# Kernel optimization log

Hardware: AMD Instinct MI355X
Metric: run time of the kernel (lower is better)

Reference implementation:

```python
import jax, jax.numpy as jnp
import numpy as np

EPS = 1e-12  # torch F.normalize eps


def setup_inputs() -> dict:
    key = jax.random.key(0)
    k1, k2, k3 = jax.random.split(key, 3)
    B, C, N, E, EMB = 128, 16, 128, 4, 16
    OUT = EMB // E  # Linear(emb_sz, emb_sz // num_edges)
    x = jax.random.normal(k1, (B, C, N, EMB), dtype=jnp.float32)
    A = jax.random.uniform(k2, (E, N, N), dtype=jnp.float32)  # non-negative adjacency
    # per-edge-type Linear weights, stored [E, in, out] so y = x @ W[e]
    W = jax.random.normal(k3, (E, EMB, OUT), dtype=jnp.float32) * (1.0 / np.sqrt(EMB))
    return {"x": x, "A": A, "W": W}


def reference(x, A, W):
    # F.normalize(A[e], dim=0): L2-normalize each column -> norm over rows (axis=1 of [E,N,N])
    col_norm = jnp.sqrt(jnp.sum(A * A, axis=1, keepdims=True))  # [E,1,N]
    An = A / jnp.maximum(col_norm, EPS)                         # [E,N,N]
    # x.transpose(3,2) @ An[e] then transpose back:
    # out[e,b,c,m,f] = sum_n x[b,c,n,f] * An[e,n,m]
    msg = jnp.einsum('bcnf,enm->ebcmf', x, An)                  # [E,B,C,N,EMB]
    # per-edge Linear (bias=False) + relu
    h = jax.nn.relu(jnp.einsum('ebcmf,efo->ebcmo', msg, W))     # [E,B,C,N,OUT]
    E_, B, C, N, O = h.shape
    # torch.cat([h_0, h_1, ...], axis=1) -> [B, E*C, N, OUT]
    out = jnp.transpose(h, (1, 0, 2, 3, 4)).reshape(B, E_ * C, N, O)
    return out
```

## Files before the change

kernel.cpp:

```cpp
#include <hip/hip_runtime.h>
#include <math.h>

#define EPSN 1e-12f

typedef __attribute__((ext_vector_type(8))) __bf16 bf16x8;
typedef __attribute__((ext_vector_type(8))) short short8;
typedef __attribute__((ext_vector_type(4))) float floatx4;

static __device__ __forceinline__ unsigned short f2bf(float f) {
    return __builtin_bit_cast(unsigned short, (__bf16)f);
}

__global__ __launch_bounds__(256)
void prep_kernel(const float* __restrict__ A, unsigned short* __restrict__ At) {
    __shared__ float Asub[128][33];
    __shared__ float red[8][32];
    __shared__ float rnv[32];
    const int t  = threadIdx.x;
    const int e  = blockIdx.x >> 2;
    const int m0 = (blockIdx.x & 3) * 32;
    const float* Ae = A + e * 16384 + m0;

    #pragma unroll
    for (int i = 0; i < 16; ++i) {
        int idx = t + i * 256;
        int n = idx >> 5, ml = idx & 31;
        Asub[n][ml] = Ae[n * 128 + ml];
    }
    __syncthreads();

    {
        int ml = t & 31, g = t >> 5;
        float s = 0.f;
        #pragma unroll
        for (int j = 0; j < 16; ++j) {
            float v = Asub[g * 16 + j][ml];
            s += v * v;
        }
        red[g][ml] = s;
    }
    __syncthreads();
    if (t < 32) {
        float s = 0.f;
        #pragma unroll
        for (int g = 0; g < 8; ++g) s += red[g][t];
        rnv[t] = 1.0f / fmaxf(sqrtf(s), EPSN);
    }
    __syncthreads();

    {
        int ml = t >> 3;
        int n0 = (t & 7) * 16;
        float r = rnv[ml];
        unsigned short hs[16];
        #pragma unroll
        for (int j = 0; j < 16; ++j)
            hs[j] = f2bf(Asub[n0 + j][ml] * r);
        uint4* dst = (uint4*)(At + ((size_t)(e * 128 + m0 + ml) * 128 + n0));
        dst[0] = *(const uint4*)&hs[0];
        dst[1] = *(const uint4*)&hs[8];
    }
}

__global__ __launch_bounds__(256)
void gcn_mfma_kernel(const float* __restrict__ x, const float* __restrict__ W,
                     const unsigned short* __restrict__ At,
                     float* __restrict__ out) {
    __shared__ __align__(16) unsigned short xw[8192];

    const int t   = threadIdx.x;
    const int bc0 = blockIdx.x * 4;

    float4 xf[2][4];
    int bcl_[2], n_[2];
    #pragma unroll
    for (int p = 0; p < 2; ++p) {
        int pair = t + p * 256;
        int bcl = pair >> 7, n = pair & 127;
        bcl_[p] = bcl; n_[p] = n;
        const float4* xp = (const float4*)(x + ((size_t)(bc0 + bcl) * 128 + n) * 16);
        xf[p][0] = xp[0]; xf[p][1] = xp[1]; xf[p][2] = xp[2]; xf[p][3] = xp[3];
    }
    #pragma unroll 1
    for (int e = 0; e < 4; ++e) {
        float4 We[16];
        const float4* wp = (const float4*)(W + e * 64);
        #pragma unroll
        for (int f = 0; f < 16; ++f) We[f] = wp[f];
        #pragma unroll
        for (int p = 0; p < 2; ++p) {
            float a0 = 0.f, a1 = 0.f, a2 = 0.f, a3 = 0.f;
            #pragma unroll
            for (int f = 0; f < 16; ++f) {
                float xv = ((const float*)&xf[p][f >> 2])[f & 3];
                a0 += xv * We[f].x; a1 += xv * We[f].y;
                a2 += xv * We[f].z; a3 += xv * We[f].w;
            }
            float av[4] = {a0, a1, a2, a3};
            int n = n_[p];
            #pragma unroll
            for (int o = 0; o < 4; ++o) {
                int r = bcl_[p] * 4 + o;
                int byteoff = (((e * 16 + r) << 8) + (n << 1)) ^ ((r & 7) << 4);
                *(unsigned short*)((char*)xw + byteoff) = f2bf(av[o]);
            }
        }
    }
    __syncthreads();

    const int e  = t >> 6;
    const int l  = t & 63;
    const int lr = l & 15;
    const int lg = l >> 4;

    bf16x8 afrag[4];
    #pragma unroll
    for (int ks = 0; ks < 4; ++ks) {
        int n0 = ks * 32 + lg * 8;
        int byteoff = (((e * 16 + lr) << 8) + (n0 << 1)) ^ ((lr & 7) << 4);
        short8 v = *(const short8*)((const char*)xw + byteoff);
        afrag[ks] = __builtin_bit_cast(bf16x8, v);
    }

    floatx4 acc[8];
    #pragma unroll
    for (int mt = 0; mt < 8; ++mt) acc[mt] = (floatx4){0.f, 0.f, 0.f, 0.f};

    const unsigned short* Ate = At + (size_t)e * 16384;
    #pragma unroll
    for (int mt = 0; mt < 8; ++mt) {
        int m = mt * 16 + lr;
        bf16x8 bfrag[4];
        #pragma unroll
        for (int ks = 0; ks < 4; ++ks) {
            int n0 = ks * 32 + lg * 8;
            short8 v = *(const short8*)(Ate + m * 128 + n0);
            bfrag[ks] = __builtin_bit_cast(bf16x8, v);
        }
        #pragma unroll
        for (int ks = 0; ks < 4; ++ks)
            acc[mt] = __builtin_amdgcn_mfma_f32_16x16x32_bf16(
                afrag[ks], bfrag[ks], acc[mt], 0, 0, 0);
    }

    const int bc = bc0 + lg, b = bc >> 4, c = bc & 15;
    float4* outp = (float4*)out + ((size_t)(b * 64 + e * 16 + c) * 128);
    #pragma unroll
    for (int mt = 0; mt < 8; ++mt) {
        int m = mt * 16 + lr;
        float4 o4;
        o4.x = fmaxf(acc[mt][0], 0.f);
        o4.y = fmaxf(acc[mt][1], 0.f);
        o4.z = fmaxf(acc[mt][2], 0.f);
        o4.w = fmaxf(acc[mt][3], 0.f);
        outp[m] = o4;
    }
}

extern "C" void kernel_launch(void* const* d_in, const int* in_sizes, int n_in,
                              void* d_out, int out_size, void* d_ws, size_t ws_size,
                              hipStream_t stream) {
    const float* x = (const float*)d_in[0];
    const float* A = (const float*)d_in[1];
    const float* W = (const float*)d_in[2];
    float* out = (float*)d_out;
    unsigned short* At = (unsigned short*)d_ws;

    prep_kernel<<<16, 256, 0, stream>>>(A, At);
    gcn_mfma_kernel<<<512, 256, 0, stream>>>(x, W, At, out);
}
```

Measured before the change: 23.10 us.

## Fuse adjacency normalization into main kernel with inter-block flag synchronization

Merges the separate prep kernel into the main MFMA kernel: the first 16 blocks normalize and transpose A into the workspace, then publish a release flag, and all blocks spin on those flags before reading At. Blocks are doubled to 512 threads handling 8 bc rows each, with each wave covering two row tiles and half the m range, so B fragments are reused across two MFMAs. This removes one kernel launch and overlaps the prep with the x@W stage, at the cost of an added memset and spin-wait that depends on the producer blocks being resident.

```diff
diff --git a/kernel.cpp b/kernel.cpp
--- a/kernel.cpp
+++ b/kernel.cpp
@@ -2,6 +2,7 @@
 #include <math.h>
 
 #define EPSN 1e-12f
+#define MAGIC 0x5A17C0DEu
 
 typedef __attribute__((ext_vector_type(8))) __bf16 bf16x8;
 typedef __attribute__((ext_vector_type(8))) short short8;
@@ -11,76 +12,79 @@
     return __builtin_bit_cast(unsigned short, (__bf16)f);
 }
 
-__global__ __launch_bounds__(256)
-void prep_kernel(const float* __restrict__ A, unsigned short* __restrict__ At) {
-    __shared__ float Asub[128][33];
-    __shared__ float red[8][32];
+__global__ __launch_bounds__(512, 2)
+void gcn_fused_kernel(const float* __restrict__ x, const float* __restrict__ A,
+                      const float* __restrict__ W,
+                      unsigned short* __restrict__ At, unsigned* __restrict__ flags,
+                      float* __restrict__ out) {
+    __shared__ __align__(16) unsigned char smem[32768];
+    __shared__ float red[16][32];
     __shared__ float rnv[32];
-    const int t  = threadIdx.x;
-    const int e  = blockIdx.x >> 2;
-    const int m0 = (blockIdx.x & 3) * 32;
-    const float* Ae = A + e * 16384 + m0;
-
-    #pragma unroll
-    for (int i = 0; i < 16; ++i) {
-        int idx = t + i * 256;
-        int n = idx >> 5, ml = idx & 31;
-        Asub[n][ml] = Ae[n * 128 + ml];
-    }
-    __syncthreads();
-
-    {
-        int ml = t & 31, g = t >> 5;
-        float s = 0.f;
-        #pragma unroll
-        for (int j = 0; j < 16; ++j) {
-            float v = Asub[g * 16 + j][ml];
-            s += v * v;
-        }
-        red[g][ml] = s;
-    }
-    __syncthreads();
-    if (t < 32) {
-        float s = 0.f;
-        #pragma unroll
-        for (int g = 0; g < 8; ++g) s += red[g][t];
-        rnv[t] = 1.0f / fmaxf(sqrtf(s), EPSN);
-    }
-    __syncthreads();
-
-    {
-        int ml = t >> 3;
-        int n0 = (t & 7) * 16;
-        float r = rnv[ml];
-        unsigned short hs[16];
-        #pragma unroll
-        for (int j = 0; j < 16; ++j)
-            hs[j] = f2bf(Asub[n0 + j][ml] * r);
-        uint4* dst = (uint4*)(At + ((size_t)(e * 128 + m0 + ml) * 128 + n0));
-        dst[0] = *(const uint4*)&hs[0];
-        dst[1] = *(const uint4*)&hs[8];
-    }
-}
-
-__global__ __launch_bounds__(256)
-void gcn_mfma_kernel(const float* __restrict__ x, const float* __restrict__ W,
-                     const unsigned short* __restrict__ At,
-                     float* __restrict__ out) {
-    __shared__ __align__(16) unsigned short xw[8192];
 
     const int t   = threadIdx.x;
-    const int bc0 = blockIdx.x * 4;
+    const int bid = blockIdx.x;
+
+    if (bid < 16) {
+        float (*Asub)[33] = (float(*)[33])smem;
+        const int ep = bid >> 2;
+        const int m0 = (bid & 3) * 32;
+        const float* Ae = A + ep * 16384 + m0;
+        #pragma unroll
+        for (int i = 0; i < 8; ++i) {
+            int idx = i * 512 + t;
+            int n = idx >> 5, ml = idx & 31;
+            Asub[n][ml] = Ae[n * 128 + ml];
+        }
+        __syncthreads();
+        {
+            int g = t >> 5, ml = t & 31;
+            float s = 0.f;
+            #pragma unroll
+            for (int j = 0; j < 8; ++j) {
+                float v = Asub[g * 8 + j][ml];
+                s += v * v;
+            }
+            red[g][ml] = s;
+        }
+        __syncthreads();
+        if (t < 32) {
+            float s = 0.f;
+            #pragma unroll
+            for (int g = 0; g < 16; ++g) s += red[g][t];
+            rnv[t] = 1.0f / fmaxf(sqrtf(s), EPSN);
+        }
+        __syncthreads();
+        {
+            int ml = t >> 4;
+            int n0 = (t & 15) * 8;
+            float r = rnv[ml];
+            unsigned short hs[8];
+            #pragma unroll
+            for (int j = 0; j < 8; ++j)
+                hs[j] = f2bf(Asub[n0 + j][ml] * r);
+            *(uint4*)(At + ((size_t)(ep * 128 + m0 + ml) * 128 + n0)) =
+                *(const uint4*)hs;
+        }
+        __threadfence();
+        __syncthreads();
+        if (t == 0)
+            __hip_atomic_store(&flags[bid], MAGIC, __ATOMIC_RELEASE,
+                               __HIP_MEMORY_SCOPE_AGENT);
+        __syncthreads();
+    }
+
+    const int bc0  = bid * 8;
+    const int bclA = t >> 7;
+    const int nn   = t & 127;
 
     float4 xf[2][4];
-    int bcl_[2], n_[2];
-    #pragma unroll
-    for (int p = 0; p < 2; ++p) {
-        int pair = t + p * 256;
-        int bcl = pair >> 7, n = pair & 127;
-        bcl_[p] = bcl; n_[p] = n;
-        const float4* xp = (const float4*)(x + ((size_t)(bc0 + bcl) * 128 + n) * 16);
-        xf[p][0] = xp[0]; xf[p][1] = xp[1]; xf[p][2] = xp[2]; xf[p][3] = xp[3];
+    {
+        const float4* xp0 = (const float4*)(x + ((size_t)(bc0 + bclA) * 128 + nn) * 16);
+        const float4* xp1 = (const float4*)(x + ((size_t)(bc0 + 4 + bclA) * 128 + nn) * 16);
+        #pragma unroll
+        for (int q = 0; q < 4; ++q) { xf[0][q] = xp0[q]; xf[1][q] = xp1[q]; }
     }
+
     #pragma unroll 1
     for (int e = 0; e < 4; ++e) {
         float4 We[16];
@@ -96,64 +100,86 @@
                 a0 += xv * We[f].x; a1 += xv * We[f].y;
                 a2 += xv * We[f].z; a3 += xv * We[f].w;
             }
-            float av[4] = {a0, a1, a2, a3};
-            int n = n_[p];
+            float av4[4] = {a0, a1, a2, a3};
+            int bcl = p * 4 + bclA;
             #pragma unroll
             for (int o = 0; o < 4; ++o) {
-                int r = bcl_[p] * 4 + o;
-                int byteoff = (((e * 16 + r) << 8) + (n << 1)) ^ ((r & 7) << 4);
-                *(unsigned short*)((char*)xw + byteoff) = f2bf(av[o]);
+                int r = bcl * 4 + o;
+                int byteoff = (((e * 32 + r) << 8) + (nn << 1)) ^ ((r & 7) << 4);
+                *(unsigned short*)(smem + byteoff) = f2bf(av4[o]);
             }
         }
     }
     __syncthreads();
 
-    const int e  = t >> 6;
-    const int l  = t & 63;
-    const int lr = l & 15;
-    const int lg = l >> 4;
+    if (t < 16) {
+        while (__hip_atomic_load(&flags[t], __ATOMIC_ACQUIRE,
+                                 __HIP_MEMORY_SCOPE_AGENT) != MAGIC)
+            __builtin_amdgcn_s_sleep(1);
+    }
+    __threadfence();
+    __syncthreads();
 
-    bf16x8 afrag[4];
+    const int wid  = t >> 6;
+    const int l    = t & 63;
+    const int e    = wid >> 1;
+    const int half = wid & 1;
+    const int lr   = l & 15;
+    const int lg   = l >> 4;
+
+    bf16x8 afrag[2][4];
     #pragma unroll
-    for (int ks = 0; ks < 4; ++ks) {
-        int n0 = ks * 32 + lg * 8;
-        int byteoff = (((e * 16 + lr) << 8) + (n0 << 1)) ^ ((lr & 7) << 4);
-        short8 v = *(const short8*)((const char*)xw + byteoff);
-        afrag[ks] = __builtin_bit_cast(bf16x8, v);
+    for (int rt = 0; rt < 2; ++rt) {
+        #pragma unroll
+        for (int ks = 0; ks < 4; ++ks) {
+            int row = rt * 16 + lr;
+            int n0 = ks * 32 + lg * 8;
+            int byteoff = (((e * 32 + row) << 8) + (n0 << 1)) ^ ((row & 7) << 4);
+            afrag[rt][ks] = __builtin_bit_cast(bf16x8, *(const short8*)(smem + byteoff));
+        }
     }
 
-    floatx4 acc[8];
+    floatx4 acc[2][4];
     #pragma unroll
-    for (int mt = 0; mt < 8; ++mt) acc[mt] = (floatx4){0.f, 0.f, 0.f, 0.f};
+    for (int rt = 0; rt < 2; ++rt)
+        #pragma unroll
+        for (int mt = 0; mt < 4; ++mt)
+            acc[rt][mt] = (floatx4){0.f, 0.f, 0.f, 0.f};
 
     const unsigned short* Ate = At + (size_t)e * 16384;
     #pragma unroll
-    for (int mt = 0; mt < 8; ++mt) {
-        int m = mt * 16 + lr;
+    for (int mt = 0; mt < 4; ++mt) {
+        int m = half * 64 + mt * 16 + lr;
         bf16x8 bfrag[4];
         #pragma unroll
         for (int ks = 0; ks < 4; ++ks) {
-            int n0 = ks * 32 + lg * 8;
-            short8 v = *(const short8*)(Ate + m * 128 + n0);
+            short8 v = *(const short8*)(Ate + (size_t)m * 128 + ks * 32 + lg * 8);
             bfrag[ks] = __builtin_bit_cast(bf16x8, v);
         }
         #pragma unroll
-        for (int ks = 0; ks < 4; ++ks)
-            acc[mt] = __builtin_amdgcn_mfma_f32_16x16x32_bf16(
-                afrag[ks], bfrag[ks], acc[mt], 0, 0, 0);
+        for (int ks = 0; ks < 4; ++ks) {
+            acc[0][mt] = __builtin_amdgcn_mfma_f32_16x16x32_bf16(
+                afrag[0][ks], bfrag[ks], acc[0][mt], 0, 0, 0);
+            acc[1][mt] = __builtin_amdgcn_mfma_f32_16x16x32_bf16(
+                afrag[1][ks], bfrag[ks], acc[1][mt], 0, 0, 0);
+        }
     }
 
-    const int bc = bc0 + lg, b = bc >> 4, c = bc & 15;
-    float4* outp = (float4*)out + ((size_t)(b * 64 + e * 16 + c) * 128);
     #pragma unroll
-    for (int mt = 0; mt < 8; ++mt) {
-        int m = mt * 16 + lr;
-        float4 o4;
-        o4.x = fmaxf(acc[mt][0], 0.f);
-        o4.y = fmaxf(acc[mt][1], 0.f);
-        o4.z = fmaxf(acc[mt][2], 0.f);
-        o4.w = fmaxf(acc[mt][3], 0.f);
-        outp[m] = o4;
+    for (int rt = 0; rt < 2; ++rt) {
+        int bc = bc0 + rt * 4 + lg;
+        int b = bc >> 4, c = bc & 15;
+        float4* outp = (float4*)out + ((size_t)(b * 64 + e * 16 + c) * 128);
+        #pragma unroll
+        for (int mt = 0; mt < 4; ++mt) {
+            int m = half * 64 + mt * 16 + lr;
+            float4 o4;
+            o4.x = fmaxf(acc[rt][mt][0], 0.f);
+            o4.y = fmaxf(acc[rt][mt][1], 0.f);
+            o4.z = fmaxf(acc[rt][mt][2], 0.f);
+            o4.w = fmaxf(acc[rt][mt][3], 0.f);
+            outp[m] = o4;
+        }
     }
 }
 
@@ -165,7 +191,8 @@
     const float* W = (const float*)d_in[2];
     float* out = (float*)d_out;
     unsigned short* At = (unsigned short*)d_ws;
+    unsigned* flags = (unsigned*)((char*)d_ws + 131072);
 
-    prep_kernel<<<16, 256, 0, stream>>>(A, At);
-    gcn_mfma_kernel<<<512, 256, 0, stream>>>(x, W, At, out);
+    hipMemsetAsync(flags, 0, 16 * sizeof(unsigned), stream);
+    gcn_fused_kernel<<<256, 512, 0, stream>>>(x, A, W, At, flags, out);
 }
```

Result: slower. 59.04 us (+155.5%).
